# Performance work log

Measured on AMD Instinct MI355X. Metric: run time of the kernel, lower is better.

## Reference

```python
import jax, jax.numpy as jnp
import numpy as np

D_MODEL = 1024
N_HEAD = 16
HEAD_DIM = D_MODEL // N_HEAD  # 64
D_FF = 4096
BATCH = 4
SEQ = 2048
EPS = 1e-5
ROPE_BASE = 10000.0


def _xavier(key, shape):
    fan_in, fan_out = shape[1], shape[0]
    limit = np.sqrt(6.0 / (fan_in + fan_out))
    return jax.random.uniform(key, shape, jnp.float32, -limit, limit)


def setup_inputs() -> dict:
    key = jax.random.key(0)
    ks = jax.random.split(key, 8)
    return {
        "src": jax.random.normal(ks[0], (BATCH, SEQ, D_MODEL), jnp.float32),
        "Wqkv": _xavier(ks[1], (3 * D_MODEL, D_MODEL)),   # torch Linear weight layout [out,in]
        "Wout": _xavier(ks[2], (D_MODEL, D_MODEL)),
        "g1": jnp.ones((D_MODEL,), jnp.float32),           # RMSNorm weights
        "g2": jnp.ones((D_MODEL,), jnp.float32),
        "W1": _xavier(ks[3], (D_FF, D_MODEL)),              # GeGLU w1
        "W2": _xavier(ks[4], (D_MODEL, D_FF)),              # GeGLU w2
        "W3": _xavier(ks[5], (D_FF, D_MODEL)),              # GeGLU w3
    }


def _rmsnorm(x, g, eps=EPS):
    return x * jax.lax.rsqrt(jnp.mean(x * x, axis=-1, keepdims=True) + eps) * g


def _rope(x):
    # x: [B, H, S, head_dim], interleaved even/odd rotation (matches torch stack+flatten)
    seq = x.shape[-2]
    inv_freq = 1.0 / (ROPE_BASE ** (jnp.arange(0, HEAD_DIM, 2, dtype=jnp.float32) / HEAD_DIM))
    t = jnp.arange(seq, dtype=jnp.float32)
    freqs = t[:, None] * inv_freq[None, :]          # [S, head_dim/2]
    cos, sin = jnp.cos(freqs), jnp.sin(freqs)
    x = x.astype(jnp.float32)
    x_even = x[..., 0::2]
    x_odd = x[..., 1::2]
    rot_even = x_even * cos - x_odd * sin
    rot_odd = x_odd * cos + x_even * sin
    return jnp.stack([rot_even, rot_odd], axis=-1).reshape(x.shape)


def reference(src, Wqkv, Wout, g1, g2, W1, W2, W3):
    B, S, _ = src.shape
    # --- attention block (pre-norm) ---
    xn = _rmsnorm(src, g1)
    qkv = xn @ Wqkv.T                                        # [B,S,3*D]
    qkv = qkv.reshape(B, S, 3, N_HEAD, HEAD_DIM).transpose(2, 0, 3, 1, 4)  # [3,B,H,S,hd]
    q, k, v = qkv[0], qkv[1], qkv[2]
    q = _rope(q)
    k = _rope(k)
    scale = 1.0 / jnp.sqrt(jnp.float32(HEAD_DIM))
    scores = jnp.einsum("bhqd,bhkd->bhqk", q, k) * scale
    probs = jax.nn.softmax(scores, axis=-1)
    attn = jnp.einsum("bhqk,bhkd->bhqd", probs, v)           # [B,H,S,hd]
    attn = attn.transpose(0, 2, 1, 3).reshape(B, S, D_MODEL)
    x = src + attn @ Wout.T
    # --- GeGLU FFN block (pre-norm) ---
    xn2 = _rmsnorm(x, g2)
    ff = (jax.nn.gelu(xn2 @ W1.T, approximate=False) * (xn2 @ W3.T)) @ W2.T
    return x + ff
```

## Files before the change

kernel.cpp:

```cpp
#include <hip/hip_runtime.h>

#define DEVI __device__ __forceinline__

typedef __attribute__((ext_vector_type(8))) short s8v;
typedef __attribute__((ext_vector_type(4))) float f4v;

DEVI unsigned short f2bf(float f) {
  unsigned int u = __float_as_uint(f);
  return (unsigned short)((u + 0x7FFFu + ((u >> 16) & 1u)) >> 16);
}
DEVI float bf2f(unsigned short h) { return __uint_as_float(((unsigned int)h) << 16); }

DEVI f4v mfma16(s8v a, s8v b, f4v c) {
  asm("v_mfma_f32_16x16x32_bf16 %0, %1, %2, %0" : "+v"(c) : "v"(a), "v"(b));
  return c;
}

DEVI float fexp2(float x) {
  float r;
  asm("v_exp_f32 %0, %1" : "=v"(r) : "v"(x));
  return r;
}

DEVI unsigned int cvtpk_bf16(float lo, float hi) {
  unsigned int r;
  asm("v_cvt_pk_bf16_f32 %0, %1, %2" : "=v"(r) : "v"(lo), "v"(hi));
  return r;
}

DEVI float gelu_t(float x) {
  const float t = x * x;
  const float a = __builtin_fmaf(t, -0.10295555f, -2.30225854f);
  return x / (1.0f + fexp2(x * a));
}

DEVI void gload_lds16(const void* g, void* l) {
  __builtin_amdgcn_global_load_lds(
      (__attribute__((address_space(1))) void*)g,
      (__attribute__((address_space(3))) void*)l, 16, 0, 0);
}

DEVI void barrier_raw() {
  asm volatile("" ::: "memory");
  __builtin_amdgcn_s_barrier();
  asm volatile("" ::: "memory");
}

DEVI void map_block(int bid, int nbx, int gw, int& by, int& bx) {
  const int xcd = bid & 7;
  const int local = bid >> 3;
  const int grp = gw * 8;
  const int q = local / grp;
  const int rem = local - q * grp;
  by = xcd * 8 + (rem & 7);
  bx = q * gw + (rem >> 3);
}

__global__ __launch_bounds__(256)
void cvt_all_k(const float* __restrict__ Wqkv, const float* __restrict__ Wout,
               const float* __restrict__ W2, const float* __restrict__ W1,
               const float* __restrict__ W3,
               unsigned short* __restrict__ wQKV, unsigned short* __restrict__ wOut,
               unsigned short* __restrict__ wW2, unsigned short* __restrict__ wI) {
  const int i = blockIdx.x * 256 + threadIdx.x;
  const float4* src;
  ushort4* dst;
  if (i < 786432) {
    src = (const float4*)Wqkv + i;
    dst = (ushort4*)wQKV + i;
  } else if (i < 1048576) {
    const int j = i - 786432;
    src = (const float4*)Wout + j;
    dst = (ushort4*)wOut + j;
  } else if (i < 2097152) {
    const int j = i - 1048576;
    src = (const float4*)W2 + j;
    dst = (ushort4*)wW2 + j;
  } else {
    const int j = i - 2097152;
    const int g = j >> 8;
    const int c4 = j & 255;
    const int srow = ((g >> 7) << 6) + (g & 63);
    const float* s = ((g >> 6) & 1) ? W3 : W1;
    src = (const float4*)(s + (size_t)srow * 1024) + c4;
    dst = (ushort4*)(wI + (size_t)g * 1024) + c4;
  }
  const float4 v = *src;
  ushort4 ov;
  ov.x = f2bf(v.x); ov.y = f2bf(v.y); ov.z = f2bf(v.z); ov.w = f2bf(v.w);
  *dst = ov;
}

__global__ __launch_bounds__(256)
void rmsnorm_k(const float* __restrict__ x, const float* __restrict__ g,
               unsigned short* __restrict__ o) {
  const int row = blockIdx.x;
  const int tid = threadIdx.x;
  const float4 v = ((const float4*)(x + (size_t)row * 1024))[tid];
  float ss = v.x * v.x + v.y * v.y + v.z * v.z + v.w * v.w;
#pragma unroll
  for (int off = 32; off > 0; off >>= 1) ss += __shfl_down(ss, off);
  __shared__ float wsum[4];
  if ((tid & 63) == 0) wsum[tid >> 6] = ss;
  __syncthreads();
  const float tot = wsum[0] + wsum[1] + wsum[2] + wsum[3];
  const float sc = rsqrtf(tot * (1.0f / 1024.0f) + 1e-5f);
  const float4 gv = ((const float4*)g)[tid];
  ushort4 ov;
  ov.x = f2bf(v.x * sc * gv.x);
  ov.y = f2bf(v.y * sc * gv.y);
  ov.z = f2bf(v.z * sc * gv.z);
  ov.w = f2bf(v.w * sc * gv.w);
  ((ushort4*)(o + (size_t)row * 1024))[tid] = ov;
}

__global__ __launch_bounds__(256)
void rope_table_k(float* __restrict__ cosT, float* __restrict__ sinT) {
  const int idx = blockIdx.x * 256 + threadIdx.x;
  const int s = idx >> 5, p = idx & 31;
  const float inv = powf(10000.0f, -(float)(2 * p) * (1.0f / 64.0f));
  const float a = (float)s * inv;
  cosT[idx] = cosf(a);
  sinT[idx] = sinf(a);
}

__global__ __launch_bounds__(256)
void vtrans_k(const unsigned short* __restrict__ v, unsigned short* __restrict__ vT) {
  __shared__ unsigned short t[64][72];
  const int bh = blockIdx.y;
  const int s0 = blockIdx.x * 64;
  const int tid = threadIdx.x;
  const int r = tid >> 3;
  const int c8 = (tid & 7) * 8;
  const unsigned short* src = v + ((size_t)bh * 2048 + s0) * 64;
#pragma unroll
  for (int it = 0; it < 2; ++it) {
    const int row = it * 32 + r;
    s8v d = *(const s8v*)(src + row * 64 + c8);
    *(s8v*)(&t[row][c8]) = d;
  }
  __syncthreads();
  unsigned short* dst = vT + (size_t)bh * 64 * 2048 + s0;
#pragma unroll
  for (int it = 0; it < 2; ++it) {
    const int d = it * 32 + r;
    s8v o;
#pragma unroll
    for (int m = 0; m < 8; ++m) o[m] = (short)t[c8 + m][d];
    *(s8v*)(dst + (size_t)d * 2048 + c8) = o;
  }
}

template <int EPI>
__global__ __launch_bounds__(256)
void gemm_bt(const unsigned short* __restrict__ A,
             const unsigned short* __restrict__ Bt,
             const int K, const int N, const int nbx, const int gw,
             unsigned short* Cb, float* Cf, const float* Xadd,
             unsigned short* __restrict__ Qp, unsigned short* __restrict__ Kp,
             unsigned short* __restrict__ Vp,
             const float* __restrict__ cosT, const float* __restrict__ sinT) {
  __shared__ __align__(16) unsigned char sA[128 * 128];
  __shared__ __align__(16) unsigned char sB[128 * 128];
  const int tid = threadIdx.x;
  const int lane = tid & 63;
  const int wave = tid >> 6;
  const int wr = (wave >> 1) * 64, wc = (wave & 1) * 64;
  int by, bx;
  map_block(blockIdx.x, nbx, gw, by, bx);
  const int row0 = by * 128;
  const int col0 = bx * 128;

  int ldsOff[4], gOffA[4], gOffB[4];
#pragma unroll
  for (int it = 0; it < 4; ++it) {
    const int p = it * 4096 + tid * 16;
    const int row = p >> 7;
    const int inner = (p & 127) ^ ((row & 7) << 4);
    ldsOff[it] = p;
    gOffA[it] = (row0 + row) * K + (inner >> 1);
    gOffB[it] = (col0 + row) * K + (inner >> 1);
  }

  f4v acc[4][4];
  const f4v fzero = {0.f, 0.f, 0.f, 0.f};
#pragma unroll
  for (int i = 0; i < 4; ++i)
#pragma unroll
    for (int j = 0; j < 4; ++j) acc[i][j] = fzero;

  const int cbase = (lane >> 4) * 16;
  const int rlane = lane & 15;

  for (int kt = 0; kt < K; kt += 64) {
    __syncthreads();
#pragma unroll
    for (int it = 0; it < 4; ++it) {
      gload_lds16(A + gOffA[it] + kt, sA + ldsOff[it]);
      gload_lds16(Bt + gOffB[it] + kt, sB + ldsOff[it]);
    }
    asm volatile("s_waitcnt vmcnt(0)" ::: "memory");
    __syncthreads();

#pragma unroll
    for (int ks = 0; ks < 2; ++ks) {
      const int cb = ks * 64 + cbase;
      s8v af[4], bfv[4];
#pragma unroll
      for (int i = 0; i < 4; ++i) {
        const int r = wr + i * 16 + rlane;
        af[i] = *(const s8v*)(sA + r * 128 + (cb ^ ((r & 7) << 4)));
      }
#pragma unroll
      for (int j = 0; j < 4; ++j) {
        const int r = wc + j * 16 + rlane;
        bfv[j] = *(const s8v*)(sB + r * 128 + (cb ^ ((r & 7) << 4)));
      }
#pragma unroll
      for (int i = 0; i < 4; ++i)
#pragma unroll
        for (int j = 0; j < 4; ++j) acc[i][j] = mfma16(af[i], bfv[j], acc[i][j]);
    }
  }

  const int rquad = (lane >> 4) * 4;

  if constexpr (EPI == 4) {
    __syncthreads();
    float* xbuf = (wave & 2) ? (float*)sB : (float*)sA;
    if (wave & 1) {
#pragma unroll
      for (int i = 0; i < 2; ++i)
#pragma unroll
        for (int j = 0; j < 4; ++j)
#pragma unroll
          for (int r = 0; r < 4; ++r)
            xbuf[((i * 16 + rquad + r) << 6) + j * 16 + rlane] = acc[i][j][r];
    } else {
#pragma unroll
      for (int i = 0; i < 2; ++i)
#pragma unroll
        for (int j = 0; j < 4; ++j)
#pragma unroll
          for (int r = 0; r < 4; ++r)
            xbuf[2048 + ((i * 16 + rquad + r) << 6) + j * 16 + rlane] = acc[2 + i][j][r];
    }
    __syncthreads();
    if (!(wave & 1)) {
#pragma unroll
      for (int i = 0; i < 2; ++i)
#pragma unroll
        for (int j = 0; j < 4; ++j)
#pragma unroll
          for (int r = 0; r < 4; ++r) {
            const int t = i * 16 + rquad + r;
            const float h1v = acc[i][j][r];
            const float h3v = xbuf[(t << 6) + j * 16 + rlane];
            Cb[(size_t)(row0 + wr + t) * N + (size_t)bx * 64 + j * 16 + rlane] =
                f2bf(gelu_t(h1v) * h3v);
          }
    } else {
#pragma unroll
      for (int i = 0; i < 2; ++i)
#pragma unroll
        for (int j = 0; j < 4; ++j)
#pragma unroll
          for (int r = 0; r < 4; ++r) {
            const int t = i * 16 + rquad + r;
            const float h1v = xbuf[2048 + (t << 6) + j * 16 + rlane];
            const float h3v = acc[2 + i][j][r];
            Cb[(size_t)(row0 + wr + 32 + t) * N + (size_t)bx * 64 + j * 16 + rlane] =
                f2bf(gelu_t(h1v) * h3v);
          }
    }
    return;
  }

#pragma unroll
  for (int i = 0; i < 4; ++i) {
#pragma unroll
    for (int j = 0; j < 4; ++j) {
#pragma unroll
      for (int r = 0; r < 4; ++r) {
        const int row = row0 + wr + i * 16 + rquad + r;
        const int col = col0 + wc + j * 16 + rlane;
        const float v = acc[i][j][r];
        if constexpr (EPI == 1) {
          const float partner = __shfl_xor(v, 1);
          const int which = col >> 10;
          const int rem = col & 1023;
          const int s = row & 2047;
          const int p = (rem & 63) >> 1;
          const float c = cosT[(s << 5) + p];
          const float sn = sinT[(s << 5) + p];
          const float sg = (rem & 1) ? sn : -sn;
          const float roped = __builtin_fmaf(partner, sg, v * c);
          const size_t idx =
              (((size_t)(row >> 11) * 16 + (rem >> 6)) * 2048 + (row & 2047)) * 64 + (rem & 63);
          if (which == 0) Qp[idx] = f2bf(roped * (0.125f * 1.44269504089f));
          else if (which == 1) Kp[idx] = f2bf(roped);
          else Vp[idx] = f2bf(v);
        } else {
          const size_t idx = (size_t)row * N + col;
          Cf[idx] = Xadd[idx] + v;
        }
      }
    }
  }
}

__global__ __launch_bounds__(256)
void attn_k(const unsigned short* __restrict__ Qg,
            const unsigned short* __restrict__ Kg,
            const unsigned short* __restrict__ VTg,
            unsigned short* __restrict__ Og) {
  __shared__ __align__(16) unsigned char sK[2][8192];
  __shared__ __align__(16) unsigned char sV[2][8192];
  __shared__ __align__(16) unsigned char sP[4][2048];

  const int tid = threadIdx.x, lane = tid & 63, wave = tid >> 6;
  int id = blockIdx.x;
  id = (id & 7) * 128 + (id >> 3);
  const int qt = id & 15, h = (id >> 4) & 15, b = id >> 8;
  const size_t bh = (size_t)b * 16 + h;
  const unsigned short* qb = Qg + (bh * 2048 + (size_t)qt * 128 + wave * 32) * 64;
  const unsigned short* kbp = Kg + bh * 2048 * 64;
  const unsigned short* vb = VTg + bh * 64 * 2048;

  const int g = lane >> 4;
  const int rl = lane & 15;
  const int cbase = g * 16;

  s8v qf[2][2];
#pragma unroll
  for (int qs = 0; qs < 2; ++qs) {
    const unsigned short* qrow = qb + (size_t)(qs * 16 + rl) * 64 + g * 8;
    qf[qs][0] = *(const s8v*)(qrow);
    qf[qs][1] = *(const s8v*)(qrow + 32);
  }

  const f4v fzero = {0.f, 0.f, 0.f, 0.f};
  f4v of[2][4];
#pragma unroll
  for (int qs = 0; qs < 2; ++qs)
#pragma unroll
    for (int jd = 0; jd < 4; ++jd) of[qs][jd] = fzero;
  float l[2] = {0.f, 0.f};

  int ldsOff[2], koff[2], voff[2];
#pragma unroll
  for (int it = 0; it < 2; ++it) {
    const int p = it * 4096 + tid * 16;
    const int row = p >> 7;
    const int inner = (p & 127) ^ ((row & 7) << 4);
    ldsOff[it] = p;
    koff[it] = row * 64 + (inner >> 1);
    voff[it] = row * 2048 + (inner >> 1);
  }

#pragma unroll
  for (int it = 0; it < 2; ++it) {
    gload_lds16(kbp + koff[it], sK[0] + ldsOff[it]);
    gload_lds16(vb + voff[it], sV[0] + ldsOff[it]);
  }

  for (int t = 0; t < 32; ++t) {
    const int buf = t & 1;
    asm volatile("s_waitcnt vmcnt(0)" ::: "memory");
    barrier_raw();
    if (t < 31) {
      const size_t kt0 = (size_t)(t + 1) * 64;
#pragma unroll
      for (int it = 0; it < 2; ++it) {
        gload_lds16(kbp + kt0 * 64 + koff[it], sK[buf ^ 1] + ldsOff[it]);
        gload_lds16(vb + kt0 + voff[it], sV[buf ^ 1] + ldsOff[it]);
      }
    }

    f4v sc[2][4];
#pragma unroll
    for (int qs = 0; qs < 2; ++qs)
#pragma unroll
      for (int jk = 0; jk < 4; ++jk) sc[qs][jk] = fzero;
    __builtin_amdgcn_s_setprio(1);
#pragma unroll
    for (int ks = 0; ks < 2; ++ks) {
      const int cb = ks * 64 + cbase;
#pragma unroll
      for (int jk = 0; jk < 4; ++jk) {
        const int r = jk * 16 + rl;
        s8v kf = *(const s8v*)(sK[buf] + r * 128 + (cb ^ ((r & 7) << 4)));
        sc[0][jk] = mfma16(kf, qf[0][ks], sc[0][jk]);
        sc[1][jk] = mfma16(kf, qf[1][ks], sc[1][jk]);
      }
    }
    __builtin_amdgcn_s_setprio(0);

#pragma unroll
    for (int qs = 0; qs < 2; ++qs) {
      float rs = 0.f;
#pragma unroll
      for (int jk = 0; jk < 4; ++jk)
#pragma unroll
        for (int mm = 0; mm < 4; ++mm) {
          const float p = fexp2(sc[qs][jk][mm]);
          sc[qs][jk][mm] = p;
          rs += p;
        }
      l[qs] += rs;
    }

    unsigned char* pbuf = sP[wave];
    s8v pa[2][2];
#pragma unroll
    for (int qs = 0; qs < 2; ++qs) {
      const int base = rl * 128;
      const int pswz = (rl & 7) << 4;
#pragma unroll
      for (int jk = 0; jk < 4; ++jk) {
        uint2 u;
        u.x = cvtpk_bf16(sc[qs][jk][0], sc[qs][jk][1]);
        u.y = cvtpk_bf16(sc[qs][jk][2], sc[qs][jk][3]);
        *(uint2*)(pbuf + base + ((32 * jk + 8 * g) ^ pswz)) = u;
      }
      pa[qs][0] = *(const s8v*)(pbuf + base + ((16 * g) ^ pswz));
      pa[qs][1] = *(const s8v*)(pbuf + base + ((64 + 16 * g) ^ pswz));
    }

    __builtin_amdgcn_s_setprio(1);
#pragma unroll
    for (int ks = 0; ks < 2; ++ks) {
      const int cb = ks * 64 + cbase;
#pragma unroll
      for (int jd = 0; jd < 4; ++jd) {
        const int r = jd * 16 + rl;
        s8v vf = *(const s8v*)(sV[buf] + r * 128 + (cb ^ ((r & 7) << 4)));
        of[0][jd] = mfma16(pa[0][ks], vf, of[0][jd]);
        of[1][jd] = mfma16(pa[1][ks], vf, of[1][jd]);
      }
    }
    __builtin_amdgcn_s_setprio(0);
  }

#pragma unroll
  for (int qs = 0; qs < 2; ++qs) {
    float lt = l[qs];
    lt += __shfl_xor(lt, 16);
    lt += __shfl_xor(lt, 32);
    const float inv = 1.0f / lt;
#pragma unroll
    for (int r = 0; r < 4; ++r) {
      const float ivr = __shfl(inv, g * 20 + r);
      const int qrow = qt * 128 + wave * 32 + qs * 16 + g * 4 + r;
      const size_t obase = ((size_t)b * 2048 + qrow) * 1024 + h * 64;
#pragma unroll
      for (int jd = 0; jd < 4; ++jd) Og[obase + jd * 16 + rl] = f2bf(of[qs][jd][r] * ivr);
    }
  }
}

extern "C" void kernel_launch(void* const* d_in, const int* in_sizes, int n_in,
                              void* d_out, int out_size, void* d_ws, size_t ws_size,
                              hipStream_t stream) {
  (void)in_sizes; (void)n_in; (void)out_size; (void)ws_size;
  const float* src  = (const float*)d_in[0];
  const float* Wqkv = (const float*)d_in[1];
  const float* Wout = (const float*)d_in[2];
  const float* g1   = (const float*)d_in[3];
  const float* g2   = (const float*)d_in[4];
  const float* W1   = (const float*)d_in[5];
  const float* W2   = (const float*)d_in[6];
  const float* W3   = (const float*)d_in[7];
  float* out = (float*)d_out;

  char* ws = (char*)d_ws;
  size_t off = 0;
  auto take = [&](size_t bytes) -> char* {
    char* p = ws + off;
    off += (bytes + 255) & ~(size_t)255;
    return p;
  };
  unsigned short* wQKV = (unsigned short*)take((size_t)3072 * 1024 * 2);
  unsigned short* wOut = (unsigned short*)take((size_t)1024 * 1024 * 2);
  unsigned short* wI   = (unsigned short*)take((size_t)8192 * 1024 * 2);
  unsigned short* wW2  = (unsigned short*)take((size_t)1024 * 4096 * 2);
  unsigned short* xn   = (unsigned short*)take((size_t)8192 * 1024 * 2);
  unsigned short* q    = (unsigned short*)take((size_t)64 * 2048 * 64 * 2);
  unsigned short* kb   = (unsigned short*)take((size_t)64 * 2048 * 64 * 2);
  unsigned short* v    = (unsigned short*)take((size_t)64 * 2048 * 64 * 2);
  unsigned short* vT   = (unsigned short*)take((size_t)64 * 64 * 2048 * 2);
  float* cosT = (float*)take((size_t)2048 * 32 * 4);
  float* sinT = (float*)take((size_t)2048 * 32 * 4);
  unsigned short* h1   = (unsigned short*)take((size_t)8192 * 4096 * 2);

  cvt_all_k<<<dim3(16384), dim3(256), 0, stream>>>(Wqkv, Wout, W2, W1, W3,
                                                   wQKV, wOut, wW2, wI);
  rope_table_k<<<dim3(2048 * 32 / 256), dim3(256), 0, stream>>>(cosT, sinT);

  rmsnorm_k<<<dim3(8192), dim3(256), 0, stream>>>(src, g1, xn);
  gemm_bt<1><<<dim3(1536), dim3(256), 0, stream>>>(xn, wQKV, 1024, 3072, 24, 8,
                                                   nullptr, nullptr, nullptr, q, kb, v, cosT, sinT);
  vtrans_k<<<dim3(32, 64), dim3(256), 0, stream>>>(v, vT);
  attn_k<<<dim3(1024), dim3(256), 0, stream>>>(q, kb, vT, xn);
  gemm_bt<3><<<dim3(512), dim3(256), 0, stream>>>(xn, wOut, 1024, 1024, 8, 4,
                                                  nullptr, out, src, nullptr, nullptr, nullptr,
                                                  nullptr, nullptr);
  rmsnorm_k<<<dim3(8192), dim3(256), 0, stream>>>(out, g2, xn);
  gemm_bt<4><<<dim3(4096), dim3(256), 0, stream>>>(xn, wI, 1024, 4096, 64, 8,
                                                   h1, nullptr, nullptr, nullptr, nullptr, nullptr,
                                                   nullptr, nullptr);
  gemm_bt<3><<<dim3(512), dim3(256), 0, stream>>>(h1, wW2, 4096, 1024, 8, 2,
                                                  nullptr, out, out, nullptr, nullptr, nullptr,
                                                  nullptr, nullptr);
}
```

Measured before the change: 469.3 us.

## Store residual in bf16 and keep attention P fragments in registers

The out-projection epilogue now writes the residual x as bf16 into the free q buffer instead of fp32. The second RMSNorm reads that bf16 copy, and the final GEMM adds it back from bf16, which cuts intermediate traffic. In the attention kernel the K rows are loaded in a permuted order, so the softmax P values can be packed directly into MFMA A-operands in registers, removing the per-wave LDS round trip. The cost is lower precision in the residual path, which adds rounding error to the output.

```diff
diff --git a/kernel.cpp b/kernel.cpp
--- a/kernel.cpp
+++ b/kernel.cpp
@@ -115,6 +115,30 @@
 }
 
 __global__ __launch_bounds__(256)
+void rmsnorm_b(const unsigned short* __restrict__ x, const float* __restrict__ g,
+               unsigned short* __restrict__ o) {
+  const int row = blockIdx.x;
+  const int tid = threadIdx.x;
+  const ushort4 hv = ((const ushort4*)(x + (size_t)row * 1024))[tid];
+  float v0 = bf2f(hv.x), v1 = bf2f(hv.y), v2 = bf2f(hv.z), v3 = bf2f(hv.w);
+  float ss = v0 * v0 + v1 * v1 + v2 * v2 + v3 * v3;
+#pragma unroll
+  for (int off = 32; off > 0; off >>= 1) ss += __shfl_down(ss, off);
+  __shared__ float wsum[4];
+  if ((tid & 63) == 0) wsum[tid >> 6] = ss;
+  __syncthreads();
+  const float tot = wsum[0] + wsum[1] + wsum[2] + wsum[3];
+  const float sc = rsqrtf(tot * (1.0f / 1024.0f) + 1e-5f);
+  const float4 gv = ((const float4*)g)[tid];
+  ushort4 ov;
+  ov.x = f2bf(v0 * sc * gv.x);
+  ov.y = f2bf(v1 * sc * gv.y);
+  ov.z = f2bf(v2 * sc * gv.z);
+  ov.w = f2bf(v3 * sc * gv.w);
+  ((ushort4*)(o + (size_t)row * 1024))[tid] = ov;
+}
+
+__global__ __launch_bounds__(256)
 void rope_table_k(float* __restrict__ cosT, float* __restrict__ sinT) {
   const int idx = blockIdx.x * 256 + threadIdx.x;
   const int s = idx >> 5, p = idx & 31;
@@ -300,9 +324,12 @@
           if (which == 0) Qp[idx] = f2bf(roped * (0.125f * 1.44269504089f));
           else if (which == 1) Kp[idx] = f2bf(roped);
           else Vp[idx] = f2bf(v);
+        } else if constexpr (EPI == 5) {
+          const size_t idx = (size_t)row * N + col;
+          Cb[idx] = f2bf(Xadd[idx] + v);
         } else {
           const size_t idx = (size_t)row * N + col;
-          Cf[idx] = Xadd[idx] + v;
+          Cf[idx] = bf2f(Qp[idx]) + v;
         }
       }
     }
@@ -316,7 +343,6 @@
             unsigned short* __restrict__ Og) {
   __shared__ __align__(16) unsigned char sK[2][8192];
   __shared__ __align__(16) unsigned char sV[2][8192];
-  __shared__ __align__(16) unsigned char sP[4][2048];
 
   const int tid = threadIdx.x, lane = tid & 63, wave = tid >> 6;
   int id = blockIdx.x;
@@ -352,9 +378,10 @@
   for (int it = 0; it < 2; ++it) {
     const int p = it * 4096 + tid * 16;
     const int row = p >> 7;
+    const int krow = (row & 32) | ((row & 12) << 1) | ((row & 16) >> 2) | (row & 3);
     const int inner = (p & 127) ^ ((row & 7) << 4);
     ldsOff[it] = p;
-    koff[it] = row * 64 + (inner >> 1);
+    koff[it] = krow * 64 + (inner >> 1);
     voff[it] = row * 2048 + (inner >> 1);
   }
 
@@ -410,21 +437,18 @@
       l[qs] += rs;
     }
 
-    unsigned char* pbuf = sP[wave];
     s8v pa[2][2];
 #pragma unroll
     for (int qs = 0; qs < 2; ++qs) {
-      const int base = rl * 128;
-      const int pswz = (rl & 7) << 4;
-#pragma unroll
-      for (int jk = 0; jk < 4; ++jk) {
-        uint2 u;
-        u.x = cvtpk_bf16(sc[qs][jk][0], sc[qs][jk][1]);
-        u.y = cvtpk_bf16(sc[qs][jk][2], sc[qs][jk][3]);
-        *(uint2*)(pbuf + base + ((32 * jk + 8 * g) ^ pswz)) = u;
-      }
-      pa[qs][0] = *(const s8v*)(pbuf + base + ((16 * g) ^ pswz));
-      pa[qs][1] = *(const s8v*)(pbuf + base + ((64 + 16 * g) ^ pswz));
+#pragma unroll
+      for (int ks = 0; ks < 2; ++ks) {
+        union { s8v v; unsigned int u[4]; } pk;
+        pk.u[0] = cvtpk_bf16(sc[qs][2 * ks][0], sc[qs][2 * ks][1]);
+        pk.u[1] = cvtpk_bf16(sc[qs][2 * ks][2], sc[qs][2 * ks][3]);
+        pk.u[2] = cvtpk_bf16(sc[qs][2 * ks + 1][0], sc[qs][2 * ks + 1][1]);
+        pk.u[3] = cvtpk_bf16(sc[qs][2 * ks + 1][2], sc[qs][2 * ks + 1][3]);
+        pa[qs][ks] = pk.v;
+      }
     }
 
     __builtin_amdgcn_s_setprio(1);
@@ -502,14 +526,14 @@
                                                    nullptr, nullptr, nullptr, q, kb, v, cosT, sinT);
   vtrans_k<<<dim3(32, 64), dim3(256), 0, stream>>>(v, vT);
   attn_k<<<dim3(1024), dim3(256), 0, stream>>>(q, kb, vT, xn);
-  gemm_bt<3><<<dim3(512), dim3(256), 0, stream>>>(xn, wOut, 1024, 1024, 8, 4,
-                                                  nullptr, out, src, nullptr, nullptr, nullptr,
+  gemm_bt<5><<<dim3(512), dim3(256), 0, stream>>>(xn, wOut, 1024, 1024, 8, 4,
+                                                  q, nullptr, src, nullptr, nullptr, nullptr,
                                                   nullptr, nullptr);
-  rmsnorm_k<<<dim3(8192), dim3(256), 0, stream>>>(out, g2, xn);
+  rmsnorm_b<<<dim3(8192), dim3(256), 0, stream>>>(q, g2, xn);
   gemm_bt<4><<<dim3(4096), dim3(256), 0, stream>>>(xn, wI, 1024, 4096, 64, 8,
                                                    h1, nullptr, nullptr, nullptr, nullptr, nullptr,
                                                    nullptr, nullptr);
-  gemm_bt<3><<<dim3(512), dim3(256), 0, stream>>>(h1, wW2, 4096, 1024, 8, 2,
-                                                  nullptr, out, out, nullptr, nullptr, nullptr,
+  gemm_bt<6><<<dim3(512), dim3(256), 0, stream>>>(h1, wW2, 4096, 1024, 8, 2,
+                                                  nullptr, out, nullptr, q, nullptr, nullptr,
                                                   nullptr, nullptr);
 }
```

New measurement: 438.0 us. 1.07x faster.
